# Kernel optimization log

Measured on AMD Instinct MI355X. Metric: run time of the kernel, lower is better.

Reference implementation:

```python
import jax, jax.numpy as jnp
import numpy as np

EPS = 1e-7  # K.epsilon()
ROUTINGS = 3

def squash(v, axis=-1):
    s2 = jnp.sum(jnp.square(v), axis=axis, keepdims=True)
    scale = s2 / (1.0 + s2) / jnp.sqrt(s2 + EPS)
    return scale * v

def setup_inputs() -> dict:
    key = jax.random.key(0)
    k1, k2 = jax.random.split(key)
    B, IN_CAPS, IN_DIM = 256, 1152, 8
    NUM_CAPS, DIM = 10, 16
    x = jax.random.normal(k1, (B, IN_CAPS, IN_DIM), dtype=jnp.float32)
    W = jax.random.normal(k2, (IN_CAPS, NUM_CAPS, IN_DIM, DIM), dtype=jnp.float32) * 0.05
    return {"x": x, "W": W}

def reference(x, W):
    # u_hat[b,i,j,d] = sum_k x[b,i,k] * W[i,j,k,d]
    u_hat = jnp.einsum('bik,ijkd->bijd', x, W)  # [B, in_caps, num_caps, dim]
    b = jnp.zeros(u_hat.shape[:-1], dtype=u_hat.dtype)  # [B, in_caps, num_caps]
    v = None
    for i in range(ROUTINGS):
        c = jax.nn.softmax(b, axis=2)                       # over num_caps
        s = jnp.einsum('bij,bijd->bjd', c, u_hat)           # [B, num_caps, dim]
        v = squash(s)
        if i < ROUTINGS - 1:
            b = b + jnp.einsum('bijd,bjd->bij', u_hat, v)   # agreement
    return v
```

## Files before the change

### kernel.cpp

```cpp
#include <hip/hip_runtime.h>
#include <cstddef>

#define B_TOT   256
#define IN_CAPS 1152
#define KDIM    8
#define NJ      10
#define ND      16
#define JD      160

#define BB      4
#define ISPLIT  8
#define IRANGE  (IN_CAPS/ISPLIT)
#define CI      16
#define IPAR    16
#define NTHREADS 640
#define NCHUNK  (IRANGE/CI)
#define WSTRIDE (NJ*KDIM*ND)
#define EPSQ    1e-7f

__device__ __forceinline__ float dot4(float4 a, float4 b) {
    return a.x*b.x + a.y*b.y + a.z*b.z + a.w*b.w;
}

template<int ITER>
__global__ __launch_bounds__(NTHREADS)
void iter_kernel(const float* __restrict__ x, const float* __restrict__ Wt,
                 const float* __restrict__ s1, const float* __restrict__ s2,
                 float* __restrict__ s_out)
{
    const int g   = blockIdx.x >> 3;
    const int isp = blockIdx.x & 7;
    const int b0  = g * BB;
    const int i_begin = isp * IRANGE;

    const int t = threadIdx.x;
    const int i_par = t / 40;
    const int r  = t - i_par * 40;
    const int j  = r >> 2;
    const int dq = r & 3;

    __shared__ float x_lds[BB][IRANGE][KDIM];
    __shared__ float logit_lds[BB][CI][NJ];
    __shared__ float c_lds[BB][CI][NJ];
    __shared__ float s_lds[BB][JD];

    float4 vs[BB];
    if (ITER >= 2) {
        #pragma unroll
        for (int bb = 0; bb < BB; ++bb) {
            const float4 a = *(const float4*)(s1 + (size_t)(b0 + bb) * JD + j * ND + dq * 4);
            float q2 = dot4(a, a);
            q2 += __shfl_xor(q2, 1);
            q2 += __shfl_xor(q2, 2);
            const float sc = q2 / (1.f + q2) / sqrtf(q2 + EPSQ);
            vs[bb] = make_float4(a.x * sc, a.y * sc, a.z * sc, a.w * sc);
            if (ITER == 3) {
                const float4 bv = *(const float4*)(s2 + (size_t)(b0 + bb) * JD + j * ND + dq * 4);
                float r2 = dot4(bv, bv);
                r2 += __shfl_xor(r2, 1);
                r2 += __shfl_xor(r2, 2);
                const float sc2 = r2 / (1.f + r2) / sqrtf(r2 + EPSQ);
                vs[bb].x += bv.x * sc2; vs[bb].y += bv.y * sc2;
                vs[bb].z += bv.z * sc2; vs[bb].w += bv.w * sc2;
            }
        }
    }

    {
        const int NF = (IRANGE * KDIM) / 4;
        for (int idx = t; idx < BB * NF; idx += NTHREADS) {
            const int bb = idx / NF;
            const int f  = idx - bb * NF;
            ((float4*)&x_lds[bb][0][0])[f] =
                ((const float4*)(x + (size_t)(b0 + bb) * IN_CAPS * KDIM
                                   + (size_t)i_begin * KDIM))[f];
        }
    }
    __syncthreads();

    float4 s_acc[BB];
    #pragma unroll
    for (int bb = 0; bb < BB; ++bb) s_acc[bb] = make_float4(0.f, 0.f, 0.f, 0.f);

    const float* wp = Wt + (size_t)((i_begin + i_par) * NJ + j) * (KDIM * ND) + dq * 4;

    for (int c = 0; c < NCHUNK; ++c) {
        const int il = c * CI + i_par;

        float4 u[BB];
        #pragma unroll
        for (int bb = 0; bb < BB; ++bb) u[bb] = make_float4(0.f, 0.f, 0.f, 0.f);
        #pragma unroll
        for (int h = 0; h < 2; ++h) {
            float xs[BB][4];
            #pragma unroll
            for (int bb = 0; bb < BB; ++bb) {
                const float4 xv = *(const float4*)&x_lds[bb][il][h * 4];
                xs[bb][0] = xv.x; xs[bb][1] = xv.y; xs[bb][2] = xv.z; xs[bb][3] = xv.w;
            }
            #pragma unroll
            for (int kk = 0; kk < 4; ++kk) {
                const float4 w4 = *(const float4*)(wp + (h * 4 + kk) * ND);
                #pragma unroll
                for (int bb = 0; bb < BB; ++bb) {
                    const float xv = xs[bb][kk];
                    u[bb].x += xv * w4.x; u[bb].y += xv * w4.y;
                    u[bb].z += xv * w4.z; u[bb].w += xv * w4.w;
                }
            }
        }

        if (ITER == 1) {
            #pragma unroll
            for (int bb = 0; bb < BB; ++bb) {
                s_acc[bb].x += u[bb].x; s_acc[bb].y += u[bb].y;
                s_acc[bb].z += u[bb].z; s_acc[bb].w += u[bb].w;
            }
        } else {
            #pragma unroll
            for (int bb = 0; bb < BB; ++bb) {
                float v = dot4(u[bb], vs[bb]);
                v += __shfl_xor(v, 1);
                v += __shfl_xor(v, 2);
                if (dq == 0) logit_lds[bb][i_par][j] = v;
            }
            __syncthreads();

            {
                const int bb  = t / (CI * NJ);
                const int rem = t - bb * (CI * NJ);
                const int il2 = rem / NJ;
                const int jj  = rem - il2 * NJ;
                float lv[NJ];
                float m = -1e30f;
                #pragma unroll
                for (int q = 0; q < NJ; ++q) {
                    lv[q] = logit_lds[bb][il2][q];
                    m = fmaxf(m, lv[q]);
                }
                float ssum = 0.f;
                #pragma unroll
                for (int q = 0; q < NJ; ++q) ssum += __expf(lv[q] - m);
                c_lds[bb][il2][jj] = __fdividef(__expf(lv[jj] - m), ssum);
            }
            __syncthreads();

            #pragma unroll
            for (int bb = 0; bb < BB; ++bb) {
                const float cc = c_lds[bb][i_par][j];
                s_acc[bb].x += cc * u[bb].x; s_acc[bb].y += cc * u[bb].y;
                s_acc[bb].z += cc * u[bb].z; s_acc[bb].w += cc * u[bb].w;
            }
        }

        wp += (size_t)CI * WSTRIDE;
    }

    ((float*)s_lds)[t] = 0.f;
    __syncthreads();
    const float premul = (ITER == 1) ? 0.1f : 1.0f;
    #pragma unroll
    for (int bb = 0; bb < BB; ++bb) {
        atomicAdd(&s_lds[bb][j * ND + dq * 4 + 0], s_acc[bb].x * premul);
        atomicAdd(&s_lds[bb][j * ND + dq * 4 + 1], s_acc[bb].y * premul);
        atomicAdd(&s_lds[bb][j * ND + dq * 4 + 2], s_acc[bb].z * premul);
        atomicAdd(&s_lds[bb][j * ND + dq * 4 + 3], s_acc[bb].w * premul);
    }
    __syncthreads();
    {
        const int bb = t / JD;
        const int jd = t - bb * JD;
        unsafeAtomicAdd(&s_out[(size_t)(b0 + bb) * JD + jd], s_lds[bb][jd]);
    }
}

__global__ __launch_bounds__(256)
void squash_kernel(const float* __restrict__ s, float* __restrict__ out)
{
    const int idx = blockIdx.x * 256 + threadIdx.x;
    const float sv = s[idx];
    float sq = sv * sv;
    sq += __shfl_xor(sq, 1);
    sq += __shfl_xor(sq, 2);
    sq += __shfl_xor(sq, 4);
    sq += __shfl_xor(sq, 8);
    const float scale = sq / (1.0f + sq) / sqrtf(sq + EPSQ);
    out[idx] = sv * scale;
}

extern "C" void kernel_launch(void* const* d_in, const int* in_sizes, int n_in,
                              void* d_out, int out_size, void* d_ws, size_t ws_size,
                              hipStream_t stream)
{
    const float* x  = (const float*)d_in[0];
    const float* Wt = (const float*)d_in[1];
    float* out = (float*)d_out;
    float* s1  = (float*)d_ws;
    float* s2  = s1 + (size_t)B_TOT * JD;
    float* s3  = s2 + (size_t)B_TOT * JD;

    hipMemsetAsync(d_ws, 0, 3 * (size_t)B_TOT * JD * sizeof(float), stream);

    dim3 grid((B_TOT / BB) * ISPLIT), blk(NTHREADS);

    iter_kernel<1><<<grid, blk, 0, stream>>>(x, Wt, nullptr, nullptr, s1);
    iter_kernel<2><<<grid, blk, 0, stream>>>(x, Wt, s1, nullptr, s2);
    iter_kernel<3><<<grid, blk, 0, stream>>>(x, Wt, s1, s2, s3);
    squash_kernel<<<dim3((B_TOT * JD) / 256), dim3(256), 0, stream>>>(s3, out);
}
```

Before: 237.8 us.

## Remap iter kernel to per-lane dim with wave-level softmax, no LDS staging

Rewrites the routing iteration kernel so that each lane owns one output dimension d and one input capsule, and loops over all 10 output capsules in registers. The softmax over capsules is now done with register shuffles inside a wave, which removes the two per-chunk block barriers and the LDS logit/coefficient buffers. x is read straight from global memory instead of being staged through LDS. Iterations 2 and 3 use 2 batches per block with 256-thread blocks, which doubles the grid. In exchange, W is read with scalar strided loads rather than float4, register pressure is higher, and W is reused across fewer batches in iterations 2 and 3.

```diff
diff --git a/kernel.cpp b/kernel.cpp
--- a/kernel.cpp
+++ b/kernel.cpp
@@ -7,170 +7,145 @@
 #define NJ      10
 #define ND      16
 #define JD      160
+#define WSTRIDE (NJ*KDIM*ND)
 
-#define BB      4
 #define ISPLIT  8
 #define IRANGE  (IN_CAPS/ISPLIT)
-#define CI      16
-#define IPAR    16
-#define NTHREADS 640
-#define NCHUNK  (IRANGE/CI)
-#define WSTRIDE (NJ*KDIM*ND)
+#define NSTEP   (IRANGE/16)
 #define EPSQ    1e-7f
 
-__device__ __forceinline__ float dot4(float4 a, float4 b) {
-    return a.x*b.x + a.y*b.y + a.z*b.z + a.w*b.w;
-}
-
 template<int ITER>
-__global__ __launch_bounds__(NTHREADS)
+__global__ __launch_bounds__(256)
 void iter_kernel(const float* __restrict__ x, const float* __restrict__ Wt,
                  const float* __restrict__ s1, const float* __restrict__ s2,
                  float* __restrict__ s_out)
 {
+    constexpr int BBK = (ITER == 1) ? 4 : 2;
+
     const int g   = blockIdx.x >> 3;
     const int isp = blockIdx.x & 7;
-    const int b0  = g * BB;
+    const int b0  = g * BBK;
     const int i_begin = isp * IRANGE;
 
-    const int t = threadIdx.x;
-    const int i_par = t / 40;
-    const int r  = t - i_par * 40;
-    const int j  = r >> 2;
-    const int dq = r & 3;
+    const int t    = threadIdx.x;
+    const int wv   = t >> 6;
+    const int lane = t & 63;
+    const int isub = (lane >> 4) & 3;
+    const int d    = lane & 15;
 
-    __shared__ float x_lds[BB][IRANGE][KDIM];
-    __shared__ float logit_lds[BB][CI][NJ];
-    __shared__ float c_lds[BB][CI][NJ];
-    __shared__ float s_lds[BB][JD];
+    __shared__ float red[4][BBK][NJ][ND];
 
-    float4 vs[BB];
-    if (ITER >= 2) {
+    float v[BBK][NJ];
+    if constexpr (ITER >= 2) {
         #pragma unroll
-        for (int bb = 0; bb < BB; ++bb) {
-            const float4 a = *(const float4*)(s1 + (size_t)(b0 + bb) * JD + j * ND + dq * 4);
-            float q2 = dot4(a, a);
-            q2 += __shfl_xor(q2, 1);
-            q2 += __shfl_xor(q2, 2);
-            const float sc = q2 / (1.f + q2) / sqrtf(q2 + EPSQ);
-            vs[bb] = make_float4(a.x * sc, a.y * sc, a.z * sc, a.w * sc);
-            if (ITER == 3) {
-                const float4 bv = *(const float4*)(s2 + (size_t)(b0 + bb) * JD + j * ND + dq * 4);
-                float r2 = dot4(bv, bv);
-                r2 += __shfl_xor(r2, 1);
-                r2 += __shfl_xor(r2, 2);
-                const float sc2 = r2 / (1.f + r2) / sqrtf(r2 + EPSQ);
-                vs[bb].x += bv.x * sc2; vs[bb].y += bv.y * sc2;
-                vs[bb].z += bv.z * sc2; vs[bb].w += bv.w * sc2;
+        for (int bb = 0; bb < BBK; ++bb) {
+            #pragma unroll
+            for (int j = 0; j < NJ; ++j) {
+                const float a = s1[(size_t)(b0 + bb) * JD + j * ND + d];
+                float q = a * a;
+                q += __shfl_xor(q, 1); q += __shfl_xor(q, 2);
+                q += __shfl_xor(q, 4); q += __shfl_xor(q, 8);
+                float vv = a * (q / (1.f + q) / sqrtf(q + EPSQ));
+                if constexpr (ITER == 3) {
+                    const float c2 = s2[(size_t)(b0 + bb) * JD + j * ND + d];
+                    float r2 = c2 * c2;
+                    r2 += __shfl_xor(r2, 1); r2 += __shfl_xor(r2, 2);
+                    r2 += __shfl_xor(r2, 4); r2 += __shfl_xor(r2, 8);
+                    vv += c2 * (r2 / (1.f + r2) / sqrtf(r2 + EPSQ));
+                }
+                v[bb][j] = vv;
             }
         }
     }
 
-    {
-        const int NF = (IRANGE * KDIM) / 4;
-        for (int idx = t; idx < BB * NF; idx += NTHREADS) {
-            const int bb = idx / NF;
-            const int f  = idx - bb * NF;
-            ((float4*)&x_lds[bb][0][0])[f] =
-                ((const float4*)(x + (size_t)(b0 + bb) * IN_CAPS * KDIM
-                                   + (size_t)i_begin * KDIM))[f];
+    float sacc[BBK][NJ];
+    #pragma unroll
+    for (int bb = 0; bb < BBK; ++bb)
+        #pragma unroll
+        for (int j = 0; j < NJ; ++j) sacc[bb][j] = 0.f;
+
+    int i = i_begin + wv * 4 + isub;
+    for (int step = 0; step < NSTEP; ++step, i += 16) {
+        float xs[BBK][KDIM];
+        #pragma unroll
+        for (int bb = 0; bb < BBK; ++bb) {
+            const float* xb = x + (size_t)(b0 + bb) * IN_CAPS * KDIM + (size_t)i * KDIM;
+            const float4 xa = *(const float4*)(xb);
+            const float4 xc = *(const float4*)(xb + 4);
+            xs[bb][0] = xa.x; xs[bb][1] = xa.y; xs[bb][2] = xa.z; xs[bb][3] = xa.w;
+            xs[bb][4] = xc.x; xs[bb][5] = xc.y; xs[bb][6] = xc.z; xs[bb][7] = xc.w;
         }
+
+        const float* wp = Wt + (size_t)i * WSTRIDE + d;
+        float u[BBK][NJ];
+        #pragma unroll
+        for (int j = 0; j < NJ; ++j) {
+            float wr[KDIM];
+            #pragma unroll
+            for (int k = 0; k < KDIM; ++k) wr[k] = wp[(j * KDIM + k) * ND];
+            #pragma unroll
+            for (int bb = 0; bb < BBK; ++bb) {
+                float acc = 0.f;
+                #pragma unroll
+                for (int k = 0; k < KDIM; ++k) acc += xs[bb][k] * wr[k];
+                u[bb][j] = acc;
+            }
+        }
+
+        if constexpr (ITER == 1) {
+            #pragma unroll
+            for (int bb = 0; bb < BBK; ++bb)
+                #pragma unroll
+                for (int j = 0; j < NJ; ++j) sacc[bb][j] += u[bb][j];
+        } else {
+            #pragma unroll
+            for (int bb = 0; bb < BBK; ++bb) {
+                float lg[NJ];
+                #pragma unroll
+                for (int j = 0; j < NJ; ++j) {
+                    float p = u[bb][j] * v[bb][j];
+                    p += __shfl_xor(p, 1); p += __shfl_xor(p, 2);
+                    p += __shfl_xor(p, 4); p += __shfl_xor(p, 8);
+                    lg[j] = p;
+                }
+                float m = lg[0];
+                #pragma unroll
+                for (int j = 1; j < NJ; ++j) m = fmaxf(m, lg[j]);
+                float ssum = 0.f;
+                #pragma unroll
+                for (int j = 0; j < NJ; ++j) { lg[j] = __expf(lg[j] - m); ssum += lg[j]; }
+                const float rinv = __fdividef(1.f, ssum);
+                #pragma unroll
+                for (int j = 0; j < NJ; ++j) sacc[bb][j] += (lg[j] * rinv) * u[bb][j];
+            }
+        }
+    }
+
+    #pragma unroll
+    for (int bb = 0; bb < BBK; ++bb)
+        #pragma unroll
+        for (int j = 0; j < NJ; ++j) {
+            float p = sacc[bb][j];
+            p += __shfl_xor(p, 16);
+            p += __shfl_xor(p, 32);
+            sacc[bb][j] = p;
+        }
+    if (lane < 16) {
+        #pragma unroll
+        for (int bb = 0; bb < BBK; ++bb)
+            #pragma unroll
+            for (int j = 0; j < NJ; ++j) red[wv][bb][j][d] = sacc[bb][j];
     }
     __syncthreads();
 
-    float4 s_acc[BB];
-    #pragma unroll
-    for (int bb = 0; bb < BB; ++bb) s_acc[bb] = make_float4(0.f, 0.f, 0.f, 0.f);
-
-    const float* wp = Wt + (size_t)((i_begin + i_par) * NJ + j) * (KDIM * ND) + dq * 4;
-
-    for (int c = 0; c < NCHUNK; ++c) {
-        const int il = c * CI + i_par;
-
-        float4 u[BB];
+    const float premul = (ITER == 1) ? 0.1f : 1.0f;
+    for (int e = t; e < BBK * JD; e += 256) {
+        const int bb  = e / JD;
+        const int rem = e - bb * JD;
+        float tot = 0.f;
         #pragma unroll
-        for (int bb = 0; bb < BB; ++bb) u[bb] = make_float4(0.f, 0.f, 0.f, 0.f);
-        #pragma unroll
-        for (int h = 0; h < 2; ++h) {
-            float xs[BB][4];
-            #pragma unroll
-            for (int bb = 0; bb < BB; ++bb) {
-                const float4 xv = *(const float4*)&x_lds[bb][il][h * 4];
-                xs[bb][0] = xv.x; xs[bb][1] = xv.y; xs[bb][2] = xv.z; xs[bb][3] = xv.w;
-            }
-            #pragma unroll
-            for (int kk = 0; kk < 4; ++kk) {
-                const float4 w4 = *(const float4*)(wp + (h * 4 + kk) * ND);
-                #pragma unroll
-                for (int bb = 0; bb < BB; ++bb) {
-                    const float xv = xs[bb][kk];
-                    u[bb].x += xv * w4.x; u[bb].y += xv * w4.y;
-                    u[bb].z += xv * w4.z; u[bb].w += xv * w4.w;
-                }
-            }
-        }
-
-        if (ITER == 1) {
-            #pragma unroll
-            for (int bb = 0; bb < BB; ++bb) {
-                s_acc[bb].x += u[bb].x; s_acc[bb].y += u[bb].y;
-                s_acc[bb].z += u[bb].z; s_acc[bb].w += u[bb].w;
-            }
-        } else {
-            #pragma unroll
-            for (int bb = 0; bb < BB; ++bb) {
-                float v = dot4(u[bb], vs[bb]);
-                v += __shfl_xor(v, 1);
-                v += __shfl_xor(v, 2);
-                if (dq == 0) logit_lds[bb][i_par][j] = v;
-            }
-            __syncthreads();
-
-            {
-                const int bb  = t / (CI * NJ);
-                const int rem = t - bb * (CI * NJ);
-                const int il2 = rem / NJ;
-                const int jj  = rem - il2 * NJ;
-                float lv[NJ];
-                float m = -1e30f;
-                #pragma unroll
-                for (int q = 0; q < NJ; ++q) {
-                    lv[q] = logit_lds[bb][il2][q];
-                    m = fmaxf(m, lv[q]);
-                }
-                float ssum = 0.f;
-                #pragma unroll
-                for (int q = 0; q < NJ; ++q) ssum += __expf(lv[q] - m);
-                c_lds[bb][il2][jj] = __fdividef(__expf(lv[jj] - m), ssum);
-            }
-            __syncthreads();
-
-            #pragma unroll
-            for (int bb = 0; bb < BB; ++bb) {
-                const float cc = c_lds[bb][i_par][j];
-                s_acc[bb].x += cc * u[bb].x; s_acc[bb].y += cc * u[bb].y;
-                s_acc[bb].z += cc * u[bb].z; s_acc[bb].w += cc * u[bb].w;
-            }
-        }
-
-        wp += (size_t)CI * WSTRIDE;
-    }
-
-    ((float*)s_lds)[t] = 0.f;
-    __syncthreads();
-    const float premul = (ITER == 1) ? 0.1f : 1.0f;
-    #pragma unroll
-    for (int bb = 0; bb < BB; ++bb) {
-        atomicAdd(&s_lds[bb][j * ND + dq * 4 + 0], s_acc[bb].x * premul);
-        atomicAdd(&s_lds[bb][j * ND + dq * 4 + 1], s_acc[bb].y * premul);
-        atomicAdd(&s_lds[bb][j * ND + dq * 4 + 2], s_acc[bb].z * premul);
-        atomicAdd(&s_lds[bb][j * ND + dq * 4 + 3], s_acc[bb].w * premul);
-    }
-    __syncthreads();
-    {
-        const int bb = t / JD;
-        const int jd = t - bb * JD;
-        unsafeAtomicAdd(&s_out[(size_t)(b0 + bb) * JD + jd], s_lds[bb][jd]);
+        for (int w = 0; w < 4; ++w) tot += (&red[w][bb][0][0])[rem];
+        unsafeAtomicAdd(&s_out[(size_t)(b0 + bb) * JD + rem], tot * premul);
     }
 }
 
@@ -201,10 +176,12 @@
 
     hipMemsetAsync(d_ws, 0, 3 * (size_t)B_TOT * JD * sizeof(float), stream);
 
-    dim3 grid((B_TOT / BB) * ISPLIT), blk(NTHREADS);
+    dim3 g1((B_TOT / 4) * ISPLIT);
+    dim3 g23((B_TOT / 2) * ISPLIT);
+    dim3 blk(256);
 
-    iter_kernel<1><<<grid, blk, 0, stream>>>(x, Wt, nullptr, nullptr, s1);
-    iter_kernel<2><<<grid, blk, 0, stream>>>(x, Wt, s1, nullptr, s2);
-    iter_kernel<3><<<grid, blk, 0, stream>>>(x, Wt, s1, s2, s3);
-    squash_kernel<<<dim3((B_TOT * JD) / 256), dim3(256), 0, stream>>>(s3, out);
+    iter_kernel<1><<<g1,  blk, 0, stream>>>(x, Wt, nullptr, nullptr, s1);
+    iter_kernel<2><<<g23, blk, 0, stream>>>(x, Wt, s1, nullptr, s2);
+    iter_kernel<3><<<g23, blk, 0, stream>>>(x, Wt, s1, s2, s3);
+    squash_kernel<<<dim3((B_TOT * JD) / 256), blk, 0, stream>>>(s3, out);
 }
```

New measurement: 201.0 us. -15.4%, faster.
